# Performance work log

Hardware: AMD Instinct MI355X
Metric: run time of the kernel (lower is better)

## Reference

```python
import jax, jax.numpy as jnp
import numpy as np

B, EMBED, HEADS, T = 2, 512, 8, 2048
DH = EMBED // HEADS
EPS = 1e-5
# NOTE: torch code computes embed_dim // num_heads ** 0.5 == 512 // sqrt(8)
SCALE = EMBED // HEADS ** 0.5  # = 181.0, reproduced faithfully


def ws_conv1x1(x, w, b, mask):
    # weight-standardized 1x1 conv; w: [O, I], x: [B, I, T], mask: [B, T]
    mu = jnp.mean(w, axis=1, keepdims=True)
    var = jnp.var(w, axis=1, keepdims=True)
    wn = (w - mu) * jax.lax.rsqrt(var + EPS)
    x = x * mask[:, None, :].astype(x.dtype)
    return jnp.einsum('oi,bit->bot', wn, x) + b[None, :, None]


def ln_head(x, g, b):
    # per-head LayerNorm over head dim; x: [B, H, DH, T], normalized over DH
    xt = jnp.swapaxes(x, -1, -2)  # [B, H, T, DH]
    mu = jnp.mean(xt, axis=-1, keepdims=True)
    var = jnp.var(xt, axis=-1, keepdims=True)
    xn = (xt - mu) * jax.lax.rsqrt(var + EPS) * g + b
    return jnp.swapaxes(xn, -1, -2)


def setup_inputs():
    key = jax.random.key(0)
    ks = jax.random.split(key, 12)
    sc = 1.0 / np.sqrt(EMBED)
    d = {
        'q': jax.random.normal(ks[0], (B, EMBED, T), jnp.float32),
        'k': jax.random.normal(ks[1], (B, EMBED, T), jnp.float32),
        'v': jax.random.normal(ks[2], (B, EMBED, T), jnp.float32),
        'query_mask': jax.random.randint(ks[3], (B, T), 0, 2, jnp.int32),
        'key_mask': jax.random.randint(ks[4], (B, T), 0, 2, jnp.int32),
        'value_mask': jax.random.randint(ks[5], (B, T), 0, 2, jnp.int32),
        'Wq': jax.random.normal(ks[6], (EMBED, EMBED), jnp.float32) * sc,
        'bq': jnp.zeros((EMBED,), jnp.float32),
        'Wk': jax.random.normal(ks[7], (EMBED, EMBED), jnp.float32) * sc,
        'bk': jnp.zeros((EMBED,), jnp.float32),
        'Wv': jax.random.normal(ks[8], (EMBED, EMBED), jnp.float32) * sc,
        'bv': jnp.zeros((EMBED,), jnp.float32),
        'Wo': jax.random.normal(ks[9], (EMBED, EMBED), jnp.float32) * sc,
        'bo': jnp.zeros((EMBED,), jnp.float32),
        'ln_gq': jnp.ones((DH,), jnp.float32), 'ln_bq': jnp.zeros((DH,), jnp.float32),
        'ln_gk': jnp.ones((DH,), jnp.float32), 'ln_bk': jnp.zeros((DH,), jnp.float32),
        'ln_gv': jnp.ones((DH,), jnp.float32), 'ln_bv': jnp.zeros((DH,), jnp.float32),
    }
    return d


def reference(q, k, v, query_mask, key_mask, value_mask,
              Wq, bq, Wk, bk, Wv, bv, Wo, bo,
              ln_gq, ln_bq, ln_gk, ln_bk, ln_gv, ln_bv):
    q = ws_conv1x1(q, Wq, bq, query_mask)   # [B, E, T]
    k = ws_conv1x1(k, Wk, bk, key_mask)
    v = ws_conv1x1(v, Wv, bv, value_mask)
    # split heads: [B, E, T] -> [B, H, DH, T]
    q = q.reshape(B, HEADS, DH, T)
    k = k.reshape(B, HEADS, DH, T)
    v = v.reshape(B, HEADS, DH, T)
    # middle_norm: per-head LayerNorm over DH
    q = ln_head(q, ln_gq, ln_bq)
    k = ln_head(k, ln_gk, ln_bk)
    v = ln_head(v, ln_gv, ln_bv)
    # scores = q^T k / scale : [B, H, Tq, Tk]
    scores = jnp.einsum('bhdq,bhdk->bhqk', q, k) / SCALE
    scores = jnp.where(key_mask[:, None, None, :] == 0, -1e9, scores)
    scores = jax.nn.softmax(scores, axis=-1)
    scores = jnp.where(query_mask[:, None, :, None] == 0, 0.0, scores)
    # out = (scores @ v^T)^T : [B, H, DH, Tq]
    out = jnp.einsum('bhqk,bhdk->bhdq', scores, v)
    out = out.reshape(B, EMBED, T)
    out = ws_conv1x1(out, Wo, bo, query_mask)
    return out
```

## Files before the change

### kernel.cpp

```cpp
#include <hip/hip_runtime.h>


typedef __bf16 bf16;
typedef __bf16 bf16x2 __attribute__((ext_vector_type(2)));
typedef __bf16 bf16x8 __attribute__((ext_vector_type(8)));
typedef _Float16 f16;
typedef _Float16 f16x8 __attribute__((ext_vector_type(8)));
typedef float  f32x4  __attribute__((ext_vector_type(4)));

#define MFMA_BF16(a, b, c) __builtin_amdgcn_mfma_f32_16x16x32_bf16((a), (b), (c), 0, 0, 0)
#define MFMA_F16_K32(a, b, c) __builtin_amdgcn_mfma_f32_16x16x32_f16((a), (b), (c), 0, 0, 0)

#if __has_builtin(__builtin_amdgcn_exp2f)
#define EXP2F(x) __builtin_amdgcn_exp2f(x)
#else
#define EXP2F(x) __expf((x) * 0.6931471805599453f)
#endif

#define NB   2
#define NE   512
#define NH   8
#define NT   2048
#define NDH  64
#define VF_BH_STRIDE (64 * 5 * 64 * 8)

__device__ __forceinline__ void gl_lds16(const bf16* g, bf16* l) {
  __builtin_amdgcn_global_load_lds(
      (const __attribute__((address_space(1))) void*)g,
      (__attribute__((address_space(3))) void*)l, 16, 0, 0);
}

__global__ __launch_bounds__(64) void k_wstd(
    const float* __restrict__ Wq, const float* __restrict__ Wk,
    const float* __restrict__ Wv, const float* __restrict__ Wo,
    bf16* __restrict__ out)
{
  const float* W = blockIdx.y == 0 ? Wq : blockIdx.y == 1 ? Wk
                 : blockIdx.y == 2 ? Wv : Wo;
  int row = blockIdx.x, lane = threadIdx.x;
  const float4* p = (const float4*)(W + row * NE) + lane * 2;
  float4 a = p[0], c = p[1];
  float s  = a.x + a.y + a.z + a.w + c.x + c.y + c.z + c.w;
  float ss = a.x*a.x + a.y*a.y + a.z*a.z + a.w*a.w
           + c.x*c.x + c.y*c.y + c.z*c.z + c.w*c.w;
#pragma unroll
  for (int m = 1; m < 64; m <<= 1) { s += __shfl_xor(s, m); ss += __shfl_xor(ss, m); }
  float mean = s * (1.0f / NE);
  float var  = ss * (1.0f / NE) - mean * mean;
  float rstd = rsqrtf(var + 1e-5f);
  bf16x8 o;
  o[0] = (bf16)((a.x - mean) * rstd); o[1] = (bf16)((a.y - mean) * rstd);
  o[2] = (bf16)((a.z - mean) * rstd); o[3] = (bf16)((a.w - mean) * rstd);
  o[4] = (bf16)((c.x - mean) * rstd); o[5] = (bf16)((c.y - mean) * rstd);
  o[6] = (bf16)((c.z - mean) * rstd); o[7] = (bf16)((c.w - mean) * rstd);
  *(bf16x8*)(out + blockIdx.y * (NE * NE) + row * NE + lane * 8) = o;
}

__global__ __launch_bounds__(256) void k_trans(
    const float* __restrict__ q, const float* __restrict__ k,
    const float* __restrict__ v,
    const int* __restrict__ qm, const int* __restrict__ km,
    const int* __restrict__ vm,
    bf16* __restrict__ xT)
{
  int src = blockIdx.z >> 1, b = blockIdx.z & 1;
  const float* x = src == 0 ? q : src == 1 ? k : v;
  const int*   m = src == 0 ? qm : src == 1 ? km : vm;
  x += (size_t)b * NE * NT;
  m += b * NT;
  int t0 = blockIdx.x * 64, i0 = blockIdx.y * 64;
  __shared__ float tile[64][65];
  int lr = threadIdx.x >> 4;
  int tc = (threadIdx.x & 15) * 4;
#pragma unroll
  for (int p = 0; p < 4; p++) {
    int row = p * 16 + lr;
    float4 v4 = *(const float4*)(x + (size_t)(i0 + row) * NT + t0 + tc);
    tile[row][tc]     = v4.x; tile[row][tc + 1] = v4.y;
    tile[row][tc + 2] = v4.z; tile[row][tc + 3] = v4.w;
  }
  __syncthreads();
  bf16* o = xT + ((size_t)src * NB + b) * NT * NE;
  int i2 = (threadIdx.x & 31) * 2, t2 = threadIdx.x >> 5;
#pragma unroll
  for (int t = t2; t < 64; t += 8) {
    float mk = (float)m[t0 + t];
    bf16x2 w2;
    w2[0] = (bf16)(tile[i2][t] * mk);
    w2[1] = (bf16)(tile[i2 + 1][t] * mk);
    *(bf16x2*)(o + (size_t)(t0 + t) * NE + i0 + i2) = w2;
  }
}

__global__ __launch_bounds__(256) void k_proj(
    const bf16* __restrict__ Wn,
    const bf16* __restrict__ xT,
    const int* __restrict__ km,
    const float* __restrict__ bq, const float* __restrict__ bk,
    const float* __restrict__ bv,
    const float* __restrict__ gq, const float* __restrict__ bbq,
    const float* __restrict__ gk, const float* __restrict__ bbk,
    const float* __restrict__ gv, const float* __restrict__ bbv,
    bf16* __restrict__ Qh, bf16* __restrict__ Kh, f16* __restrict__ Vf)
{
  int src = blockIdx.z >> 1, b = blockIdx.z & 1;
  const bf16* A  = Wn + src * (NE * NE);
  const bf16* Bm = xT + ((size_t)src * NB + b) * NT * NE;
  int m0 = blockIdx.y * 64, n0 = blockIdx.x * 128;
  int h = m0 >> 6;

  __shared__ __align__(16) char smem[49152];
  bf16*  Al = (bf16*)smem;
  bf16*  Bl = (bf16*)(smem + 16384);
  float* Yl = (float*)smem;
  float* mu = (float*)(smem + 64 * 130 * 4);
  float* rs = mu + 128;

  int tid = threadIdx.x, lane = tid & 63, w = tid >> 6;
  int mh = (w & 1) * 32, nh = (w >> 1) * 64;
  int lr4 = lane >> 4, c16 = lane & 15;
  f32x4 acc[2][4] = {};

  for (int k0 = 0; k0 < NE; k0 += 128) {
    __syncthreads();
#pragma unroll
    for (int i = 0; i < 4; i++) {
      int row = w * 16 + i * 4 + lr4;
      gl_lds16(A + (m0 + row) * NE + k0 + ((c16 ^ (row & 15)) << 3),
               Al + (w * 16 + i * 4) * 128);
    }
#pragma unroll
    for (int i = 0; i < 8; i++) {
      int row = w * 32 + i * 4 + lr4;
      gl_lds16(Bm + (size_t)(n0 + row) * NE + k0 + ((c16 ^ (row & 15)) << 3),
               Bl + (w * 32 + i * 4) * 128);
    }
    __syncthreads();
#pragma unroll
    for (int kk = 0; kk < 128; kk += 32) {
      bf16x8 af[2], bfv[4];
#pragma unroll
      for (int ms = 0; ms < 2; ms++) {
        int row = mh + ms * 16 + (lane & 15);
        int slot = ((kk >> 3) + (lane >> 4)) ^ (row & 15);
        af[ms] = *(const bf16x8*)(Al + row * 128 + (slot << 3));
      }
#pragma unroll
      for (int ns = 0; ns < 4; ns++) {
        int row = nh + ns * 16 + (lane & 15);
        int slot = ((kk >> 3) + (lane >> 4)) ^ (row & 15);
        bfv[ns] = *(const bf16x8*)(Bl + row * 128 + (slot << 3));
      }
#pragma unroll
      for (int ms = 0; ms < 2; ms++)
#pragma unroll
        for (int ns = 0; ns < 4; ns++)
          acc[ms][ns] = MFMA_BF16(af[ms], bfv[ns], acc[ms][ns]);
    }
  }

  __syncthreads();
  {
    const float* bias = src == 0 ? bq : src == 1 ? bk : bv;
#pragma unroll
    for (int ms = 0; ms < 2; ms++)
#pragma unroll
      for (int ns = 0; ns < 4; ns++)
#pragma unroll
        for (int r = 0; r < 4; r++) {
          int om = mh + ms * 16 + ((lane >> 4) << 2) + r;
          int on = nh + ns * 16 + (lane & 15);
          Yl[om * 130 + on] = acc[ms][ns][r] + bias[m0 + om];
        }
  }
  __syncthreads();
  if (tid < 128) {
    float s = 0.f, ss = 0.f;
#pragma unroll 8
    for (int o = 0; o < 64; o++) { float y = Yl[o * 130 + tid]; s += y; ss += y * y; }
    float mean = s * (1.0f / 64.0f);
    float var  = ss * (1.0f / 64.0f) - mean * mean;
    mu[tid] = mean;
    rs[tid] = rsqrtf(var + 1e-5f);
  }
  __syncthreads();

  if (src < 2) {
    float scl = (src == 0) ? (1.4426950408889634f / 181.0f) : 1.0f;
    const float* g  = src == 0 ? gq  : gk;
    const float* bb = src == 0 ? bbq : bbk;
    bf16* out = (src == 0 ? Qh : Kh) + ((size_t)(b * NH + h) * NT + n0) * NDH;
    int d2 = (tid & 31) * 2, tb2 = tid >> 5;
    float g0 = g[d2] * scl,     b0 = bb[d2] * scl;
    float g1 = g[d2 + 1] * scl, b1 = bb[d2 + 1] * scl;
#pragma unroll
    for (int t = tb2; t < 128; t += 8) {
      float rmu = mu[t], rrs = rs[t];
      bf16x2 w2;
      w2[0] = (bf16)((Yl[d2 * 130 + t] - rmu) * rrs * g0 + b0);
      w2[1] = (bf16)((Yl[(d2 + 1) * 130 + t] - rmu) * rrs * g1 + b1);
      *(bf16x2*)(out + (size_t)t * NDH + d2) = w2;
    }
  } else {
    int gl = tid >> 6, lane2 = tid & 63;
    int quad2 = lane2 >> 4, l15b = lane2 & 15;
    int bh = b * NH + h;
    f16* base = Vf + (size_t)bh * VF_BH_STRIDE
              + (size_t)((n0 >> 5) + gl) * (5 * 64 * 8) + lane2 * 8;
    int   tl[8]; float mk[8];
#pragma unroll
    for (int j = 0; j < 8; j++) {
      tl[j] = gl * 32 + ((j < 4) ? quad2 * 4 + j : 16 + quad2 * 4 + (j - 4));
      mk[j] = (float)km[b * NT + n0 + tl[j]];
    }
#pragma unroll
    for (int ds = 0; ds < 4; ds++) {
      int d = ds * 16 + l15b;
      float gg = gv[d], bb3 = bbv[d];
      f16x8 o;
#pragma unroll
      for (int j = 0; j < 8; j++) {
        int t = tl[j];
        o[j] = (f16)(((Yl[d * 130 + t] - mu[t]) * rs[t] * gg + bb3) * mk[j]);
      }
      *(f16x8*)(base + ds * (64 * 8)) = o;
    }
    f16x8 om;
#pragma unroll
    for (int j = 0; j < 8; j++) om[j] = (f16)mk[j];
    *(f16x8*)(base + 4 * (64 * 8)) = om;
  }
}

struct KV {
  bf16x8 ka[2][2];
  f16x8  vb[5];
};

__device__ __forceinline__ void kv_load(KV& s, const bf16* Kb, const f16* VfW,
                                        int kk) {
#pragma unroll
  for (int kt = 0; kt < 2; kt++)
#pragma unroll
    for (int hf = 0; hf < 2; hf++)
      s.ka[kt][hf] = *(const bf16x8*)(Kb + (size_t)(kk + kt * 16) * NDH + hf * 32);
  const f16* vp = VfW + (size_t)(kk >> 5) * (5 * 512);
#pragma unroll
  for (int j5 = 0; j5 < 5; j5++)
    s.vb[j5] = *(const f16x8*)(vp + j5 * 512);
}

__device__ __forceinline__ void kv_comp(const KV& s, const bf16x8 qb[4][2],
                                        f32x4 acco[4][4], f32x4 dacc[4]) {
#pragma unroll
  for (int qs = 0; qs < 4; qs++) {
    f32x4 z0 = {}, z1 = {};
    z0 = MFMA_BF16(s.ka[0][0], qb[qs][0], z0);
    z0 = MFMA_BF16(s.ka[0][1], qb[qs][1], z0);
    z1 = MFMA_BF16(s.ka[1][0], qb[qs][0], z1);
    z1 = MFMA_BF16(s.ka[1][1], qb[qs][1], z1);
    f16x8 pa;
#pragma unroll
    for (int r = 0; r < 4; r++) {
      pa[r]     = (f16)EXP2F(z0[r]);
      pa[4 + r] = (f16)EXP2F(z1[r]);
    }
    dacc[qs] = MFMA_F16_K32(pa, s.vb[4], dacc[qs]);
#pragma unroll
    for (int ds = 0; ds < 4; ds++)
      acco[qs][ds] = MFMA_F16_K32(pa, s.vb[ds], acco[qs][ds]);
  }
}

__global__ __launch_bounds__(256) void k_attn(
    const bf16* __restrict__ Qh, const bf16* __restrict__ Kh,
    const f16* __restrict__ Vf, const int* __restrict__ qmask,
    bf16* __restrict__ xa)
{
  int bh = blockIdx.y, b = bh >> 3, h = bh & 7;
  int q0 = blockIdx.x * 64;
  const bf16* Q = Qh + (size_t)bh * NT * NDH;
  const bf16* K = Kh + (size_t)bh * NT * NDH;
  const f16*  VfB = Vf + (size_t)bh * VF_BH_STRIDE;

  __shared__ __align__(16) char smem[2 * 64 * 68 * 4 + 4 * 64 * 4];
  float* OlA  = (float*)smem;
  float* OlB  = (float*)(smem + 64 * 68 * 4);
  float* denl = (float*)(smem + 2 * 64 * 68 * 4);

  int tid = threadIdx.x, lane = tid & 63, w = tid >> 6;
  int quad = lane >> 4, l15 = lane & 15;
  const int ko = w * 32;

  bf16x8 qb[4][2];
#pragma unroll
  for (int qs = 0; qs < 4; qs++)
#pragma unroll
    for (int hf = 0; hf < 2; hf++)
      qb[qs][hf] = *(const bf16x8*)(Q + (size_t)(q0 + qs * 16 + l15) * NDH + hf * 32 + quad * 8);

  const bf16* Kb  = K + (size_t)(ko + l15) * NDH + quad * 8;
  const f16*  VfW = VfB + (size_t)w * (5 * 512) + lane * 8;

  f32x4 acco[4][4] = {};
  f32x4 dacc[4]    = {};

  KV s0, s1;
  kv_load(s0, Kb, VfW, 0);
  kv_load(s1, Kb, VfW, 128);

#pragma unroll
  for (int i = 0; i < 8; i++) {
    KV n0, n1;
    if (i < 7) kv_load(n0, Kb, VfW, i * 256 + 256);
    kv_comp(s0, qb, acco, dacc);
    if (i < 7) kv_load(n1, Kb, VfW, i * 256 + 384);
    kv_comp(s1, qb, acco, dacc);
    if (i < 7) { s0 = n0; s1 = n1; }
  }

  if (l15 == 0)
#pragma unroll
    for (int qs = 0; qs < 4; qs++)
#pragma unroll
      for (int r = 0; r < 4; r++)
        denl[w * 64 + qs * 16 + quad * 4 + r] = dacc[qs][r];

  float* Obuf = (w < 2) ? OlA : OlB;
  if ((w & 1) == 0) {
#pragma unroll
    for (int qs = 0; qs < 4; qs++)
#pragma unroll
      for (int ds = 0; ds < 4; ds++)
#pragma unroll
        for (int r = 0; r < 4; r++)
          Obuf[(qs * 16 + quad * 4 + r) * 68 + ds * 16 + l15] = acco[qs][ds][r];
  }
  __syncthreads();
  if (w & 1) {
#pragma unroll
    for (int qs = 0; qs < 4; qs++)
#pragma unroll
      for (int ds = 0; ds < 4; ds++)
#pragma unroll
        for (int r = 0; r < 4; r++)
          Obuf[(qs * 16 + quad * 4 + r) * 68 + ds * 16 + l15] += acco[qs][ds][r];
  }
  __syncthreads();

#pragma unroll
  for (int i = 0; i < 16; i++) {
    int ql = w * 16 + i;
    float dtot = denl[ql] + denl[64 + ql] + denl[128 + ql] + denl[192 + ql];
    float qm = (float)qmask[b * NT + q0 + ql];
    float inv = qm / dtot;
    float val = (OlA[ql * 68 + lane] + OlB[ql * 68 + lane]) * inv;
    xa[((size_t)b * NT + q0 + ql) * NE + h * NDH + lane] = (bf16)val;
  }
}

__global__ __launch_bounds__(256) void k_oproj(
    const bf16* __restrict__ A,
    const bf16* __restrict__ xab,
    const float* __restrict__ bo, float* __restrict__ out)
{
  int b = blockIdx.z;
  const bf16* Bm = xab + (size_t)b * NT * NE;
  int m0 = blockIdx.y * 64, n0 = blockIdx.x * 64;

  __shared__ __align__(16) char smem[32768];
  bf16* Al = (bf16*)smem;
  bf16* Bl = (bf16*)(smem + 16384);

  int tid = threadIdx.x, lane = tid & 63, w = tid >> 6;
  int mh = (w & 1) * 32, nh = (w >> 1) * 32;
  int lr4 = lane >> 4, c16 = lane & 15;
  f32x4 acc[2][2] = {};

  for (int k0 = 0; k0 < NE; k0 += 128) {
    __syncthreads();
#pragma unroll
    for (int i = 0; i < 4; i++) {
      int row = w * 16 + i * 4 + lr4;
      gl_lds16(A + (m0 + row) * NE + k0 + ((c16 ^ (row & 15)) << 3),
               Al + (w * 16 + i * 4) * 128);
    }
#pragma unroll
    for (int i = 0; i < 4; i++) {
      int row = w * 16 + i * 4 + lr4;
      gl_lds16(Bm + (size_t)(n0 + row) * NE + k0 + ((c16 ^ (row & 15)) << 3),
               Bl + (w * 16 + i * 4) * 128);
    }
    __syncthreads();
#pragma unroll
    for (int kk = 0; kk < 128; kk += 32) {
      bf16x8 af[2], bfv[2];
#pragma unroll
      for (int ms = 0; ms < 2; ms++) {
        int row = mh + ms * 16 + (lane & 15);
        int slot = ((kk >> 3) + (lane >> 4)) ^ (row & 15);
        af[ms] = *(const bf16x8*)(Al + row * 128 + (slot << 3));
      }
#pragma unroll
      for (int ns = 0; ns < 2; ns++) {
        int row = nh + ns * 16 + (lane & 15);
        int slot = ((kk >> 3) + (lane >> 4)) ^ (row & 15);
        bfv[ns] = *(const bf16x8*)(Bl + row * 128 + (slot << 3));
      }
#pragma unroll
      for (int ms = 0; ms < 2; ms++)
#pragma unroll
        for (int ns = 0; ns < 2; ns++)
          acc[ms][ns] = MFMA_BF16(af[ms], bfv[ns], acc[ms][ns]);
    }
  }

#pragma unroll
  for (int ms = 0; ms < 2; ms++)
#pragma unroll
    for (int ns = 0; ns < 2; ns++)
#pragma unroll
      for (int r = 0; r < 4; r++) {
        int o = m0 + mh + ms * 16 + ((lane >> 4) << 2) + r;
        int t = n0 + nh + ns * 16 + (lane & 15);
        out[(size_t)b * NE * NT + (size_t)o * NT + t] = acc[ms][ns][r] + bo[o];
      }
}

extern "C" void kernel_launch(void* const* d_in, const int* in_sizes, int n_in,
                              void* d_out, int out_size, void* d_ws, size_t ws_size,
                              hipStream_t stream)
{
  const float* q  = (const float*)d_in[0];
  const float* k  = (const float*)d_in[1];
  const float* v  = (const float*)d_in[2];
  const int*   qm = (const int*)d_in[3];
  const int*   km = (const int*)d_in[4];
  const int*   vm = (const int*)d_in[5];
  const float* Wq = (const float*)d_in[6];  const float* bq = (const float*)d_in[7];
  const float* Wk = (const float*)d_in[8];  const float* bk = (const float*)d_in[9];
  const float* Wv = (const float*)d_in[10]; const float* bv = (const float*)d_in[11];
  const float* Wo = (const float*)d_in[12]; const float* bo = (const float*)d_in[13];
  const float* gq = (const float*)d_in[14]; const float* bbq = (const float*)d_in[15];
  const float* gk = (const float*)d_in[16]; const float* bbk = (const float*)d_in[17];
  const float* gv = (const float*)d_in[18]; const float* bbv = (const float*)d_in[19];
  float* out = (float*)d_out;

  char* wsb = (char*)d_ws;
  bf16*  Wn  = (bf16*)(wsb);
  bf16*  xT  = (bf16*)(wsb + (2ull  << 20));
  bf16*  xa  = (bf16*)(wsb + (2ull  << 20));
  bf16*  Qh  = (bf16*)(wsb + (14ull << 20));
  bf16*  Kh  = (bf16*)(wsb + (18ull << 20));
  f16*   Vf  = (f16*) (wsb + (22ull << 20));

  k_wstd <<<dim3(512, 4),   64,  0, stream>>>(Wq, Wk, Wv, Wo, Wn);
  k_trans<<<dim3(32, 8, 6), 256, 0, stream>>>(q, k, v, qm, km, vm, xT);
  k_proj <<<dim3(16, 8, 6), 256, 0, stream>>>(Wn, xT, km, bq, bk, bv,
                                              gq, bbq, gk, bbk, gv, bbv,
                                              Qh, Kh, Vf);
  k_attn <<<dim3(32, 16),   256, 0, stream>>>(Qh, Kh, Vf, qm, xa);
  k_oproj<<<dim3(32, 8, 2), 256, 0, stream>>>(Wn + 3 * NE * NE, xa, bo, out);
}
```

Before: 156.6 us.

## Split attention over key halves, merge weight-std into transpose, parallelize LN stats

Attention is split across two key ranges (grid z=2), so each block handles 1024 keys. Each block writes unnormalized fp16 partial outputs plus per-query denominators, and a new combine kernel sums the two halves, applies the query mask and normalizes to bf16. The aim is to double the number of attention blocks and fill more CUs. The weight-standardization kernel is folded into the transpose kernel as an extra z-slice, saving one launch. The LayerNorm statistics in k_proj now use all 256 threads via two partial sums. The cost is an extra launch and extra global traffic for the partials, plus fp16 rounding of the unnormalized partial sums.

New measurement: 164.1 us. +4.8%, slower.

```diff
diff --git a/kernel.cpp b/kernel.cpp
--- a/kernel.cpp
+++ b/kernel.cpp
@@ -30,48 +30,51 @@
       (__attribute__((address_space(3))) void*)l, 16, 0, 0);
 }
 
-__global__ __launch_bounds__(64) void k_wstd(
-    const float* __restrict__ Wq, const float* __restrict__ Wk,
-    const float* __restrict__ Wv, const float* __restrict__ Wo,
-    bf16* __restrict__ out)
-{
-  const float* W = blockIdx.y == 0 ? Wq : blockIdx.y == 1 ? Wk
-                 : blockIdx.y == 2 ? Wv : Wo;
-  int row = blockIdx.x, lane = threadIdx.x;
-  const float4* p = (const float4*)(W + row * NE) + lane * 2;
-  float4 a = p[0], c = p[1];
-  float s  = a.x + a.y + a.z + a.w + c.x + c.y + c.z + c.w;
-  float ss = a.x*a.x + a.y*a.y + a.z*a.z + a.w*a.w
-           + c.x*c.x + c.y*c.y + c.z*c.z + c.w*c.w;
-#pragma unroll
-  for (int m = 1; m < 64; m <<= 1) { s += __shfl_xor(s, m); ss += __shfl_xor(ss, m); }
-  float mean = s * (1.0f / NE);
-  float var  = ss * (1.0f / NE) - mean * mean;
-  float rstd = rsqrtf(var + 1e-5f);
-  bf16x8 o;
-  o[0] = (bf16)((a.x - mean) * rstd); o[1] = (bf16)((a.y - mean) * rstd);
-  o[2] = (bf16)((a.z - mean) * rstd); o[3] = (bf16)((a.w - mean) * rstd);
-  o[4] = (bf16)((c.x - mean) * rstd); o[5] = (bf16)((c.y - mean) * rstd);
-  o[6] = (bf16)((c.z - mean) * rstd); o[7] = (bf16)((c.w - mean) * rstd);
-  *(bf16x8*)(out + blockIdx.y * (NE * NE) + row * NE + lane * 8) = o;
-}
-
-__global__ __launch_bounds__(256) void k_trans(
+__global__ __launch_bounds__(256) void k_pre(
     const float* __restrict__ q, const float* __restrict__ k,
     const float* __restrict__ v,
     const int* __restrict__ qm, const int* __restrict__ km,
     const int* __restrict__ vm,
-    bf16* __restrict__ xT)
+    const float* __restrict__ Wq, const float* __restrict__ Wk,
+    const float* __restrict__ Wv, const float* __restrict__ Wo,
+    bf16* __restrict__ xT, bf16* __restrict__ Wn)
 {
+  __shared__ float tile[64][65];
+  int tid = threadIdx.x;
+  if (blockIdx.z == 6) {
+    int id = blockIdx.y * 32 + blockIdx.x;
+    int w = tid >> 6, lane = tid & 63;
+#pragma unroll
+    for (int r = 0; r < 2; r++) {
+      int rg  = id * 8 + w * 2 + r;
+      int mat = rg >> 9, row = rg & 511;
+      const float* W = mat == 0 ? Wq : mat == 1 ? Wk : mat == 2 ? Wv : Wo;
+      const float4* p = (const float4*)(W + row * NE) + lane * 2;
+      float4 a = p[0], c = p[1];
+      float s  = a.x + a.y + a.z + a.w + c.x + c.y + c.z + c.w;
+      float ss = a.x*a.x + a.y*a.y + a.z*a.z + a.w*a.w
+               + c.x*c.x + c.y*c.y + c.z*c.z + c.w*c.w;
+#pragma unroll
+      for (int m = 1; m < 64; m <<= 1) { s += __shfl_xor(s, m); ss += __shfl_xor(ss, m); }
+      float mean = s * (1.0f / NE);
+      float var  = ss * (1.0f / NE) - mean * mean;
+      float rstd = rsqrtf(var + 1e-5f);
+      bf16x8 o;
+      o[0] = (bf16)((a.x - mean) * rstd); o[1] = (bf16)((a.y - mean) * rstd);
+      o[2] = (bf16)((a.z - mean) * rstd); o[3] = (bf16)((a.w - mean) * rstd);
+      o[4] = (bf16)((c.x - mean) * rstd); o[5] = (bf16)((c.y - mean) * rstd);
+      o[6] = (bf16)((c.z - mean) * rstd); o[7] = (bf16)((c.w - mean) * rstd);
+      *(bf16x8*)(Wn + (size_t)rg * NE + lane * 8) = o;
+    }
+    return;
+  }
   int src = blockIdx.z >> 1, b = blockIdx.z & 1;
   const float* x = src == 0 ? q : src == 1 ? k : v;
   const int*   m = src == 0 ? qm : src == 1 ? km : vm;
   x += (size_t)b * NE * NT;
   m += b * NT;
   int t0 = blockIdx.x * 64, i0 = blockIdx.y * 64;
-  __shared__ float tile[64][65];
-  int lr = threadIdx.x >> 4;
-  int tc = (threadIdx.x & 15) * 4;
+  int lr = tid >> 4, tc = (tid & 15) * 4;
 #pragma unroll
   for (int p = 0; p < 4; p++) {
     int row = p * 16 + lr;
@@ -81,7 +84,7 @@
   }
   __syncthreads();
   bf16* o = xT + ((size_t)src * NB + b) * NT * NE;
-  int i2 = (threadIdx.x & 31) * 2, t2 = threadIdx.x >> 5;
+  int i2 = (tid & 31) * 2, t2 = tid >> 5;
 #pragma unroll
   for (int t = t2; t < 64; t += 8) {
     float mk = (float)m[t0 + t];
@@ -113,8 +116,10 @@
   bf16*  Al = (bf16*)smem;
   bf16*  Bl = (bf16*)(smem + 16384);
   float* Yl = (float*)smem;
-  float* mu = (float*)(smem + 64 * 130 * 4);
-  float* rs = mu + 128;
+  float* mu = (float*)(smem + 33280);
+  float* rs = (float*)(smem + 33792);
+  float* ps = (float*)(smem + 34304);
+  float* pq = (float*)(smem + 35328);
 
   int tid = threadIdx.x, lane = tid & 63, w = tid >> 6;
   int mh = (w & 1) * 32, nh = (w >> 1) * 64;
@@ -174,10 +179,19 @@
         }
   }
   __syncthreads();
-  if (tid < 128) {
+  {
+    int c = tid & 127, hh = tid >> 7;
     float s = 0.f, ss = 0.f;
 #pragma unroll 8
-    for (int o = 0; o < 64; o++) { float y = Yl[o * 130 + tid]; s += y; ss += y * y; }
+    for (int o = hh * 32; o < hh * 32 + 32; o++) {
+      float y = Yl[o * 130 + c]; s += y; ss += y * y;
+    }
+    ps[hh * 128 + c] = s; pq[hh * 128 + c] = ss;
+  }
+  __syncthreads();
+  if (tid < 128) {
+    float s  = ps[tid] + ps[128 + tid];
+    float ss = pq[tid] + pq[128 + tid];
     float mean = s * (1.0f / 64.0f);
     float var  = ss * (1.0f / 64.0f) - mean * mean;
     mu[tid] = mean;
@@ -274,11 +288,13 @@
 
 __global__ __launch_bounds__(256) void k_attn(
     const bf16* __restrict__ Qh, const bf16* __restrict__ Kh,
-    const f16* __restrict__ Vf, const int* __restrict__ qmask,
-    bf16* __restrict__ xa)
+    const f16* __restrict__ Vf,
+    f16* __restrict__ Op,
+    float* __restrict__ Dens)
 {
   int bh = blockIdx.y, b = bh >> 3, h = bh & 7;
   int q0 = blockIdx.x * 64;
+  int z  = blockIdx.z, zb = z * 1024;
   const bf16* Q = Qh + (size_t)bh * NT * NDH;
   const bf16* K = Kh + (size_t)bh * NT * NDH;
   const f16*  VfB = Vf + (size_t)bh * VF_BH_STRIDE;
@@ -299,8 +315,9 @@
     for (int hf = 0; hf < 2; hf++)
       qb[qs][hf] = *(const bf16x8*)(Q + (size_t)(q0 + qs * 16 + l15) * NDH + hf * 32 + quad * 8);
 
-  const bf16* Kb  = K + (size_t)(ko + l15) * NDH + quad * 8;
-  const f16*  VfW = VfB + (size_t)w * (5 * 512) + lane * 8;
+  const bf16* Kb  = K + (size_t)(zb + ko + l15) * NDH + quad * 8;
+  const f16*  VfW = VfB + (size_t)(zb >> 5) * (5 * 512)
+                  + (size_t)w * (5 * 512) + lane * 8;
 
   f32x4 acco[4][4] = {};
   f32x4 dacc[4]    = {};
@@ -310,13 +327,13 @@
   kv_load(s1, Kb, VfW, 128);
 
 #pragma unroll
-  for (int i = 0; i < 8; i++) {
+  for (int i = 0; i < 4; i++) {
     KV n0, n1;
-    if (i < 7) kv_load(n0, Kb, VfW, i * 256 + 256);
+    if (i < 3) kv_load(n0, Kb, VfW, i * 256 + 256);
     kv_comp(s0, qb, acco, dacc);
-    if (i < 7) kv_load(n1, Kb, VfW, i * 256 + 384);
+    if (i < 3) kv_load(n1, Kb, VfW, i * 256 + 384);
     kv_comp(s1, qb, acco, dacc);
-    if (i < 7) { s0 = n0; s1 = n1; }
+    if (i < 3) { s0 = n0; s1 = n1; }
   }
 
   if (l15 == 0)
@@ -348,15 +365,39 @@
   }
   __syncthreads();
 
+  f16*   OpZ = Op + (size_t)z * NB * NT * NE;
+  float* DnZ = Dens + (size_t)z * NB * NH * NT;
 #pragma unroll
   for (int i = 0; i < 16; i++) {
     int ql = w * 16 + i;
-    float dtot = denl[ql] + denl[64 + ql] + denl[128 + ql] + denl[192 + ql];
-    float qm = (float)qmask[b * NT + q0 + ql];
-    float inv = qm / dtot;
-    float val = (OlA[ql * 68 + lane] + OlB[ql * 68 + lane]) * inv;
-    xa[((size_t)b * NT + q0 + ql) * NE + h * NDH + lane] = (bf16)val;
-  }
+    float val = OlA[ql * 68 + lane] + OlB[ql * 68 + lane];
+    OpZ[((size_t)b * NT + q0 + ql) * NE + h * NDH + lane] = (f16)val;
+    if (lane == 0) {
+      float dtot = denl[ql] + denl[64 + ql] + denl[128 + ql] + denl[192 + ql];
+      DnZ[(size_t)bh * NT + q0 + ql] = dtot;
+    }
+  }
+}
+
+__global__ __launch_bounds__(256) void k_comb(
+    const f16* __restrict__ Op, const float* __restrict__ Dens,
+    const int* __restrict__ qmask, bf16* __restrict__ xa)
+{
+  int row = blockIdx.x * 4 + (threadIdx.x >> 6);
+  int e8  = (threadIdx.x & 63) * 8;
+  int b = row >> 11, t = row & (NT - 1), h = e8 >> 6;
+  const f16* p0 = Op + (size_t)row * NE + e8;
+  const f16* p1 = p0 + (size_t)NB * NT * NE;
+  f16x8 a = *(const f16x8*)p0;
+  f16x8 c = *(const f16x8*)p1;
+  float d = Dens[(size_t)(b * NH + h) * NT + t]
+          + Dens[(size_t)NB * NH * NT + (size_t)(b * NH + h) * NT + t];
+  float inv = (float)qmask[row] / d;
+  bf16x8 o;
+#pragma unroll
+  for (int j = 0; j < 8; j++)
+    o[j] = (bf16)(((float)a[j] + (float)c[j]) * inv);
+  *(bf16x8*)(xa + (size_t)row * NE + e8) = o;
 }
 
 __global__ __launch_bounds__(256) void k_oproj(
@@ -449,16 +490,19 @@
   char* wsb = (char*)d_ws;
   bf16*  Wn  = (bf16*)(wsb);
   bf16*  xT  = (bf16*)(wsb + (2ull  << 20));
-  bf16*  xa  = (bf16*)(wsb + (2ull  << 20));
+  f16*   Op  = (f16*) (wsb + (2ull  << 20));
+  float* Dns = (float*)(wsb + (2ull  << 20) + (10ull << 20) + (512ull << 10));
   bf16*  Qh  = (bf16*)(wsb + (14ull << 20));
   bf16*  Kh  = (bf16*)(wsb + (18ull << 20));
   f16*   Vf  = (f16*) (wsb + (22ull << 20));
-
-  k_wstd <<<dim3(512, 4),   64,  0, stream>>>(Wq, Wk, Wv, Wo, Wn);
-  k_trans<<<dim3(32, 8, 6), 256, 0, stream>>>(q, k, v, qm, km, vm, xT);
-  k_proj <<<dim3(16, 8, 6), 256, 0, stream>>>(Wn, xT, km, bq, bk, bv,
-                                              gq, bbq, gk, bbk, gv, bbv,
-                                              Qh, Kh, Vf);
-  k_attn <<<dim3(32, 16),   256, 0, stream>>>(Qh, Kh, Vf, qm, xa);
-  k_oproj<<<dim3(32, 8, 2), 256, 0, stream>>>(Wn + 3 * NE * NE, xa, bo, out);
-}
+  bf16*  xa  = (bf16*)(wsb + (28ull << 20));
+
+  k_pre  <<<dim3(32, 8, 7),  256, 0, stream>>>(q, k, v, qm, km, vm,
+                                               Wq, Wk, Wv, Wo, xT, Wn);
+  k_proj <<<dim3(16, 8, 6),  256, 0, stream>>>(Wn, xT, km, bq, bk, bv,
+                                               gq, bbq, gk, bbk, gv, bbv,
+                                               Qh, Kh, Vf);
+  k_attn <<<dim3(32, 16, 2), 256, 0, stream>>>(Qh, Kh, Vf, Op, Dns);
+  k_comb <<<dim3(1024),      256, 0, stream>>>(Op, Dns, qm, xa);
+  k_oproj<<<dim3(32, 8, 2),  256, 0, stream>>>(Wn + 3 * NE * NE, xa, bo, out);
+}
```

## Fuse weight standardization into transpose kernel and deepen attention KV prefetch

Applied to the files above, without the earlier changes.

Merges the weight-standardization kernel into the input transpose/mask kernel as an extra z-slice of blocks, which removes one kernel launch. In the projection epilogue, the per-column LayerNorm statistics now use all 256 threads: each half sums 32 rows and the partial sums are combined through LDS. The attention KV loop changes from two-slot double buffering to a three-deep rolling prefetch over 128-key chunks, so loads are issued further ahead of compute. The deeper prefetch keeps one more KV buffer live in registers, which raises register pressure.

Measured after the change: 156.5 us. About the same (-0.1%).

```diff
diff --git a/kernel.cpp b/kernel.cpp
--- a/kernel.cpp
+++ b/kernel.cpp
@@ -30,48 +30,51 @@
       (__attribute__((address_space(3))) void*)l, 16, 0, 0);
 }
 
-__global__ __launch_bounds__(64) void k_wstd(
-    const float* __restrict__ Wq, const float* __restrict__ Wk,
-    const float* __restrict__ Wv, const float* __restrict__ Wo,
-    bf16* __restrict__ out)
-{
-  const float* W = blockIdx.y == 0 ? Wq : blockIdx.y == 1 ? Wk
-                 : blockIdx.y == 2 ? Wv : Wo;
-  int row = blockIdx.x, lane = threadIdx.x;
-  const float4* p = (const float4*)(W + row * NE) + lane * 2;
-  float4 a = p[0], c = p[1];
-  float s  = a.x + a.y + a.z + a.w + c.x + c.y + c.z + c.w;
-  float ss = a.x*a.x + a.y*a.y + a.z*a.z + a.w*a.w
-           + c.x*c.x + c.y*c.y + c.z*c.z + c.w*c.w;
-#pragma unroll
-  for (int m = 1; m < 64; m <<= 1) { s += __shfl_xor(s, m); ss += __shfl_xor(ss, m); }
-  float mean = s * (1.0f / NE);
-  float var  = ss * (1.0f / NE) - mean * mean;
-  float rstd = rsqrtf(var + 1e-5f);
-  bf16x8 o;
-  o[0] = (bf16)((a.x - mean) * rstd); o[1] = (bf16)((a.y - mean) * rstd);
-  o[2] = (bf16)((a.z - mean) * rstd); o[3] = (bf16)((a.w - mean) * rstd);
-  o[4] = (bf16)((c.x - mean) * rstd); o[5] = (bf16)((c.y - mean) * rstd);
-  o[6] = (bf16)((c.z - mean) * rstd); o[7] = (bf16)((c.w - mean) * rstd);
-  *(bf16x8*)(out + blockIdx.y * (NE * NE) + row * NE + lane * 8) = o;
-}
-
-__global__ __launch_bounds__(256) void k_trans(
+__global__ __launch_bounds__(256) void k_pre(
     const float* __restrict__ q, const float* __restrict__ k,
     const float* __restrict__ v,
     const int* __restrict__ qm, const int* __restrict__ km,
     const int* __restrict__ vm,
-    bf16* __restrict__ xT)
+    const float* __restrict__ Wq, const float* __restrict__ Wk,
+    const float* __restrict__ Wv, const float* __restrict__ Wo,
+    bf16* __restrict__ xT, bf16* __restrict__ Wn)
 {
+  __shared__ float tile[64][65];
+  int tid = threadIdx.x;
+  if (blockIdx.z == 6) {
+    int id = blockIdx.y * 32 + blockIdx.x;
+    int w = tid >> 6, lane = tid & 63;
+#pragma unroll
+    for (int r = 0; r < 2; r++) {
+      int rg  = id * 8 + w * 2 + r;
+      int mat = rg >> 9, row = rg & 511;
+      const float* W = mat == 0 ? Wq : mat == 1 ? Wk : mat == 2 ? Wv : Wo;
+      const float4* p = (const float4*)(W + row * NE) + lane * 2;
+      float4 a = p[0], c = p[1];
+      float s  = a.x + a.y + a.z + a.w + c.x + c.y + c.z + c.w;
+      float ss = a.x*a.x + a.y*a.y + a.z*a.z + a.w*a.w
+               + c.x*c.x + c.y*c.y + c.z*c.z + c.w*c.w;
+#pragma unroll
+      for (int m = 1; m < 64; m <<= 1) { s += __shfl_xor(s, m); ss += __shfl_xor(ss, m); }
+      float mean = s * (1.0f / NE);
+      float var  = ss * (1.0f / NE) - mean * mean;
+      float rstd = rsqrtf(var + 1e-5f);
+      bf16x8 o;
+      o[0] = (bf16)((a.x - mean) * rstd); o[1] = (bf16)((a.y - mean) * rstd);
+      o[2] = (bf16)((a.z - mean) * rstd); o[3] = (bf16)((a.w - mean) * rstd);
+      o[4] = (bf16)((c.x - mean) * rstd); o[5] = (bf16)((c.y - mean) * rstd);
+      o[6] = (bf16)((c.z - mean) * rstd); o[7] = (bf16)((c.w - mean) * rstd);
+      *(bf16x8*)(Wn + (size_t)rg * NE + lane * 8) = o;
+    }
+    return;
+  }
   int src = blockIdx.z >> 1, b = blockIdx.z & 1;
   const float* x = src == 0 ? q : src == 1 ? k : v;
   const int*   m = src == 0 ? qm : src == 1 ? km : vm;
   x += (size_t)b * NE * NT;
   m += b * NT;
   int t0 = blockIdx.x * 64, i0 = blockIdx.y * 64;
-  __shared__ float tile[64][65];
-  int lr = threadIdx.x >> 4;
-  int tc = (threadIdx.x & 15) * 4;
+  int lr = tid >> 4, tc = (tid & 15) * 4;
 #pragma unroll
   for (int p = 0; p < 4; p++) {
     int row = p * 16 + lr;
@@ -81,7 +84,7 @@
   }
   __syncthreads();
   bf16* o = xT + ((size_t)src * NB + b) * NT * NE;
-  int i2 = (threadIdx.x & 31) * 2, t2 = threadIdx.x >> 5;
+  int i2 = (tid & 31) * 2, t2 = tid >> 5;
 #pragma unroll
   for (int t = t2; t < 64; t += 8) {
     float mk = (float)m[t0 + t];
@@ -113,8 +116,10 @@
   bf16*  Al = (bf16*)smem;
   bf16*  Bl = (bf16*)(smem + 16384);
   float* Yl = (float*)smem;
-  float* mu = (float*)(smem + 64 * 130 * 4);
-  float* rs = mu + 128;
+  float* mu = (float*)(smem + 33280);
+  float* rs = (float*)(smem + 33792);
+  float* ps = (float*)(smem + 34304);
+  float* pq = (float*)(smem + 35328);
 
   int tid = threadIdx.x, lane = tid & 63, w = tid >> 6;
   int mh = (w & 1) * 32, nh = (w >> 1) * 64;
@@ -174,10 +179,19 @@
         }
   }
   __syncthreads();
-  if (tid < 128) {
+  {
+    int c = tid & 127, hh = tid >> 7;
     float s = 0.f, ss = 0.f;
 #pragma unroll 8
-    for (int o = 0; o < 64; o++) { float y = Yl[o * 130 + tid]; s += y; ss += y * y; }
+    for (int o = hh * 32; o < hh * 32 + 32; o++) {
+      float y = Yl[o * 130 + c]; s += y; ss += y * y;
+    }
+    ps[hh * 128 + c] = s; pq[hh * 128 + c] = ss;
+  }
+  __syncthreads();
+  if (tid < 128) {
+    float s  = ps[tid] + ps[128 + tid];
+    float ss = pq[tid] + pq[128 + tid];
     float mean = s * (1.0f / 64.0f);
     float var  = ss * (1.0f / 64.0f) - mean * mean;
     mu[tid] = mean;
@@ -305,18 +319,17 @@
   f32x4 acco[4][4] = {};
   f32x4 dacc[4]    = {};
 
-  KV s0, s1;
+  KV s0, s1, s2;
   kv_load(s0, Kb, VfW, 0);
   kv_load(s1, Kb, VfW, 128);
-
-#pragma unroll
-  for (int i = 0; i < 8; i++) {
-    KV n0, n1;
-    if (i < 7) kv_load(n0, Kb, VfW, i * 256 + 256);
+  kv_load(s2, Kb, VfW, 256);
+
+#pragma unroll
+  for (int c = 0; c < 16; c++) {
+    KV n;
+    if (c < 13) kv_load(n, Kb, VfW, c * 128 + 384);
     kv_comp(s0, qb, acco, dacc);
-    if (i < 7) kv_load(n1, Kb, VfW, i * 256 + 384);
-    kv_comp(s1, qb, acco, dacc);
-    if (i < 7) { s0 = n0; s1 = n1; }
+    s0 = s1; s1 = s2; s2 = n;
   }
 
   if (l15 == 0)
@@ -454,8 +467,8 @@
   bf16*  Kh  = (bf16*)(wsb + (18ull << 20));
   f16*   Vf  = (f16*) (wsb + (22ull << 20));
 
-  k_wstd <<<dim3(512, 4),   64,  0, stream>>>(Wq, Wk, Wv, Wo, Wn);
-  k_trans<<<dim3(32, 8, 6), 256, 0, stream>>>(q, k, v, qm, km, vm, xT);
+  k_pre  <<<dim3(32, 8, 7), 256, 0, stream>>>(q, k, v, qm, km, vm,
+                                              Wq, Wk, Wv, Wo, xT, Wn);
   k_proj <<<dim3(16, 8, 6), 256, 0, stream>>>(Wn, xT, km, bq, bk, bv,
                                               gq, bbq, gk, bbk, gv, bbv,
                                               Qh, Kh, Vf);
```
